# Performance work log

Hardware: AMD Instinct MI355X
Metric: run time of the kernel (lower is better)

## Reference

```python
import jax, jax.numpy as jnp
import numpy as np

B, S, DIM = 2, 4096, 768
G = DIM // 3          # gate_dim = 256
H, DK = 4, G // 4     # heads=4, d_k=64
SCALE = 1.0 / np.sqrt(DK)


def setup_inputs() -> dict:
    key = jax.random.key(0)
    ks = jax.random.split(key, 9)
    r = lambda k, shp, s: (jax.random.normal(k, shp, dtype=jnp.float32) * s)
    w_s = 1.0 / np.sqrt(G)
    return {
        "x": r(ks[0], (B, S, DIM), 1.0),
        "wq": r(ks[1], (G, G), w_s), "bq": r(ks[2], (G,), 0.01),
        "wk": r(ks[3], (G, G), w_s), "bk": r(ks[4], (G,), 0.01),
        "wv": r(ks[5], (G, G), w_s), "bv": r(ks[6], (G,), 0.01),
        "wo": r(ks[7], (G, G), w_s), "bo": r(ks[8], (G,), 0.01),
    }


def reference(x, wq, bq, wk, bk, wv, bv, wo, bo):
    # chunk(3, dim=-1): q/k/v slices of width G
    xq, xk, xv = x[..., :G], x[..., G:2 * G], x[..., 2 * G:3 * G]
    # linear projections then split into heads: [b, s, h, d]
    q = (xq @ wq.T + bq).reshape(B, S, H, DK)
    k = (xk @ wk.T + bk).reshape(B, S, H, DK)
    v = (xv @ wv.T + bv).reshape(B, S, H, DK)
    scores = jnp.einsum('bihd,bjhd->bijh', q, k) * SCALE  # [b, i, j, h]
    # NOTE: original applies Softmax(dim=1) -> over the QUERY axis i
    attn = jax.nn.softmax(scores, axis=1)
    out = jnp.einsum('bijh,bjhd->bihd', attn, v).reshape(B, S, G)
    return out @ wo.T + bo
```

## Files before the change

kernel.cpp:

```cpp
#include <hip/hip_runtime.h>

#define SEQ   4096
#define HH    4
#define SCALE 0.125f
#define SC2   0.18033688011112042f
#define C16   -23.083120654223414f

typedef __bf16 bf16x8 __attribute__((ext_vector_type(8)));
typedef __bf16 bf16x4 __attribute__((ext_vector_type(4)));
typedef float  f32x4  __attribute__((ext_vector_type(4)));

constexpr size_t OFF_W16  = 0;
constexpr size_t OFF_A    = 131072;
constexpr size_t OFF_AO   = 294912;
constexpr size_t OFF_X16  = 9732096;
constexpr size_t OFF_Q16  = 12877824;
constexpr size_t K16OFF   = 2097152;
constexpr size_t V16OFF   = 4194304;
constexpr size_t OFF_PZ   = 16023552;

__device__ __forceinline__ f32x4 mf(bf16x8 a, bf16x8 b, f32x4 c) {
    return __builtin_amdgcn_mfma_f32_16x16x32_bf16(a, b, c, 0, 0, 0);
}

__device__ __forceinline__ void gload16(const __bf16* g, __bf16* l) {
    __builtin_amdgcn_global_load_lds(
        (const __attribute__((address_space(1))) unsigned int*)g,
        (__attribute__((address_space(3))) unsigned int*)l, 16, 0, 0);
}

__device__ __forceinline__ float ex2(float x) {
    return __builtin_amdgcn_exp2f(x);
}

__global__ void k_prep(const float* __restrict__ x,
                       const float* __restrict__ wq, const float* __restrict__ wk,
                       const float* __restrict__ wv, const float* __restrict__ wo,
                       float* __restrict__ ws) {
    int bx = blockIdx.x, t = threadIdx.x;
    if (bx < 6144) {
        size_t i4 = ((size_t)bx * 256 + t) * 4;
        float4 v = *(const float4*)(x + i4);
        bf16x4 o = {(__bf16)v.x, (__bf16)v.y, (__bf16)v.z, (__bf16)v.w};
        *(bf16x4*)((__bf16*)(ws + OFF_X16) + i4) = o;
    } else if (bx < 6400) {
        int q = bx - 6144;
        int y = q >> 6;
        const float* src = (y == 0) ? wq : (y == 1) ? wk : (y == 2) ? wv : wo;
        size_t i4 = ((size_t)(q & 63) * 256 + t) * 4;
        float4 v = *(const float4*)(src + i4);
        bf16x4 o = {(__bf16)v.x, (__bf16)v.y, (__bf16)v.z, (__bf16)v.w};
        *(bf16x4*)((__bf16*)(ws + OFF_W16) + (size_t)y * 65536 + i4) = o;
    } else {
        size_t i4 = ((size_t)(bx - 6400) * 256 + t) * 4;
        *(float4*)(ws + OFF_AO + i4) = make_float4(0.f, 0.f, 0.f, 0.f);
    }
}

__global__ __launch_bounds__(256) void k_qkv_mfma(const float* __restrict__ bq,
                                                  const float* __restrict__ bk,
                                                  const float* __restrict__ bv,
                                                  float* __restrict__ ws) {
    int t = threadIdx.x, lane = t & 63, w = t >> 6;
    int yw = blockIdx.y;
    int row0 = blockIdx.x * 64 + w * 16;
    int mrow = lane & 15, quad = lane >> 4;
    const __bf16* X16 = (const __bf16*)(ws + OFF_X16);
    const __bf16* W16 = (const __bf16*)(ws + OFF_W16) + (size_t)yw * 65536;
    const float* bias = (yw == 0) ? bq : (yw == 1) ? bk : bv;
    __bf16* Qb = (__bf16*)(ws + OFF_Q16);
    f32x4 acc[16];
#pragma unroll
    for (int n = 0; n < 16; n++) acc[n] = {0.f, 0.f, 0.f, 0.f};
    const __bf16* ap = X16 + (size_t)(row0 + mrow) * 768 + yw * 256 + quad * 8;
    const __bf16* bp = W16 + (size_t)mrow * 256 + quad * 8;
    for (int kc = 0; kc < 256; kc += 32) {
        bf16x8 a = *(const bf16x8*)(ap + kc);
#pragma unroll
        for (int nt = 0; nt < 16; nt++) {
            bf16x8 b = *(const bf16x8*)(bp + (size_t)nt * 16 * 256 + kc);
            acc[nt] = mf(a, b, acc[nt]);
        }
    }
#pragma unroll
    for (int nt = 0; nt < 16; nt++) {
        int n = nt * 16 + mrow;
        float bb = bias[n];
        int h = n >> 6, d = n & 63;
#pragma unroll
        for (int r = 0; r < 4; r++) {
            int sg = row0 + quad * 4 + r;
            int b_ = sg >> 12, s = sg & 4095;
            int bh = b_ * HH + h;
            float val = acc[nt][r] + bb;
            if (yw == 0) {
                int tile = s >> 4, m = s & 15, frag = d >> 5, q2 = (d >> 3) & 3, e = d & 7;
                size_t idx = (((size_t)bh * 256 + tile) * 2 + frag) * 512 +
                             (size_t)(q2 * 16 + m) * 8 + e;
                Qb[idx] = (__bf16)val;
            } else if (yw == 1) {
                int jc = s >> 5, jj = s & 31;
                int tl = (jj >> 2) & 1, m = ((jj >> 3) << 2) | (jj & 3);
                int frag = d >> 5, q2 = (d >> 3) & 3, e = d & 7;
                size_t idx = (((size_t)bh * 128 + jc) * 4 + tl * 2 + frag) * 512 +
                             (size_t)(q2 * 16 + m) * 8 + e;
                Qb[K16OFF + idx] = (__bf16)val;
            } else {
                int jc = s >> 5, qk = (s >> 3) & 3, e = s & 7;
                int nd = d >> 4, nl = d & 15;
                size_t idx = (((size_t)bh * 128 + jc) * 4 + nd) * 512 +
                             (size_t)(qk * 16 + nl) * 8 + e;
                Qb[V16OFF + idx] = (__bf16)val;
            }
        }
    }
}

__global__ __launch_bounds__(256) void k_colstats(float* __restrict__ ws) {
    __shared__ __bf16 qbuf[2][4096];
    int t = threadIdx.x, lane = t & 63, w = t >> 6;
    int jb = blockIdx.x, iy = blockIdx.y, bh = blockIdx.z;
    int jc = jb * 4 + w;
    const __bf16* Qp = (const __bf16*)(ws + OFF_Q16);
    const __bf16* Kp = Qp + K16OFF;
    const __bf16* kb = Kp + ((size_t)(bh * 128 + jc) * 4) * 512 + lane * 8;
    bf16x8 bk00 = *(const bf16x8*)(kb);
    bf16x8 bk01 = *(const bf16x8*)(kb + 512);
    bf16x8 bk10 = *(const bf16x8*)(kb + 1024);
    bf16x8 bk11 = *(const bf16x8*)(kb + 1536);
    const __bf16* q0 = Qp + ((size_t)(bh * 256 + iy * 32) * 2) * 512 +
                       w * 1024 + lane * 8;
    gload16(q0, qbuf[0] + w * 1024);
    gload16(q0 + 512, qbuf[0] + w * 1024 + 512);
    __syncthreads();
    float z0 = 0.f, z1 = 0.f;
    for (int ic = 0; ic < 8; ic++) {
        const __bf16* cur = qbuf[ic & 1];
        if (ic < 7) {
            const __bf16* qn = Qp + ((size_t)(bh * 256 + iy * 32 + (ic + 1) * 4) * 2) * 512 +
                               w * 1024 + lane * 8;
            gload16(qn, qbuf[(ic + 1) & 1] + w * 1024);
            gload16(qn + 512, qbuf[(ic + 1) & 1] + w * 1024 + 512);
        }
#pragma unroll
        for (int it = 0; it < 4; it++) {
            bf16x8 a0 = *(const bf16x8*)(cur + it * 1024 + lane * 8);
            bf16x8 a1 = *(const bf16x8*)(cur + it * 1024 + 512 + lane * 8);
            f32x4 c0 = {0.f, 0.f, 0.f, 0.f};
            c0 = mf(a0, bk00, c0);
            c0 = mf(a1, bk01, c0);
            f32x4 c1 = {0.f, 0.f, 0.f, 0.f};
            c1 = mf(a0, bk10, c1);
            c1 = mf(a1, bk11, c1);
#pragma unroll
            for (int r = 0; r < 4; r++) {
                z0 += ex2(fmaf(c0[r], SC2, C16));
                z1 += ex2(fmaf(c1[r], SC2, C16));
            }
        }
        __syncthreads();
    }
    z0 += __shfl_xor(z0, 16, 64);
    z0 += __shfl_xor(z0, 32, 64);
    z1 += __shfl_xor(z1, 16, 64);
    z1 += __shfl_xor(z1, 32, 64);
    if (lane < 16) {
        size_t o = OFF_PZ + (size_t)iy * 32768 + (size_t)bh * SEQ +
                   jc * 32 + ((lane >> 2) << 3) + (lane & 3);
        ws[o] = z0;
        ws[o + 4] = z1;
    }
}

__global__ void k_afin(float* __restrict__ ws) {
    int idx = blockIdx.x * 256 + threadIdx.x;
    const float* pz = ws + OFF_PZ;
    float Z = 0.f;
#pragma unroll
    for (int y = 0; y < 8; y++) Z += pz[(size_t)y * 32768 + idx];
    ws[OFF_A + idx] = C16 - __log2f(Z);
}

__global__ __launch_bounds__(256) void k_attnpv(float* __restrict__ ws) {
    __shared__ __align__(16) char pool[20480];
    __bf16* ldsK = (__bf16*)pool;
    __bf16* ldsV = (__bf16*)(pool + 8192);
    float*  sA   = (float*)(pool + 16384);
    int t = threadIdx.x, lane = t & 63, w = t >> 6;
    int jy = blockIdx.y, bh = blockIdx.z;
    int it0 = blockIdx.x * 4 + w;
    int i0 = it0 * 16;
    int mrow = lane & 15, quad = lane >> 4;
    const __bf16* Qp = (const __bf16*)(ws + OFF_Q16);
    const __bf16* Kp = Qp + K16OFF;
    const __bf16* Vp = Qp + V16OFF;
    int jbase = jy * 1024;
    {
        const float* Ag = ws + OFF_A + (size_t)bh * SEQ + jbase;
        *(float4*)(sA + t * 4) = *(const float4*)(Ag + t * 4);
    }
    const __bf16* qb = Qp + ((size_t)(bh * 256 + it0) * 2) * 512 + lane * 8;
    bf16x8 aq0 = *(const bf16x8*)(qb);
    bf16x8 aq1 = *(const bf16x8*)(qb + 512);
    f32x4 oaccT[4];
#pragma unroll
    for (int nd = 0; nd < 4; nd++) oaccT[nd] = {0.f, 0.f, 0.f, 0.f};
    int c0g = jy * 32;
    {
        const __bf16* kg = Kp + ((size_t)(bh * 128 + c0g) * 4) * 512 + w * 512 + lane * 8;
        gload16(kg, ldsK + w * 512);
        const __bf16* vg = Vp + ((size_t)(bh * 128 + c0g) * 4) * 512 + w * 512 + lane * 8;
        gload16(vg, ldsV + w * 512);
    }
    __syncthreads();

    for (int jt = 0; jt < 32; jt++) {
        const __bf16* curK = ldsK + (jt & 1) * 2048;
        const __bf16* curV = ldsV + (jt & 1) * 2048;
        if (jt < 31) {
            int cn = c0g + jt + 1;
            const __bf16* kg = Kp + ((size_t)(bh * 128 + cn) * 4) * 512 + w * 512 + lane * 8;
            gload16(kg, ldsK + ((jt + 1) & 1) * 2048 + w * 512);
            const __bf16* vg = Vp + ((size_t)(bh * 128 + cn) * 4) * 512 + w * 512 + lane * 8;
            gload16(vg, ldsV + ((jt + 1) & 1) * 2048 + w * 512);
        }
        f32x4 a4L = *(const f32x4*)(sA + jt * 32 + quad * 8);
        f32x4 a4H = *(const f32x4*)(sA + jt * 32 + quad * 8 + 4);
        bf16x8 ck0 = *(const bf16x8*)(curK + lane * 8);
        bf16x8 ck1 = *(const bf16x8*)(curK + 512 + lane * 8);
        bf16x8 ck2 = *(const bf16x8*)(curK + 1024 + lane * 8);
        bf16x8 ck3 = *(const bf16x8*)(curK + 1536 + lane * 8);
        f32x4 cT0 = {0.f, 0.f, 0.f, 0.f};
        cT0 = mf(ck0, aq0, cT0);
        cT0 = mf(ck1, aq1, cT0);
        f32x4 cT1 = {0.f, 0.f, 0.f, 0.f};
        cT1 = mf(ck2, aq0, cT1);
        cT1 = mf(ck3, aq1, cT1);
        bf16x8 pb;
#pragma unroll
        for (int r = 0; r < 4; r++) {
            pb[r]     = (__bf16)ex2(fmaf(cT0[r], SC2, a4L[r]));
            pb[4 + r] = (__bf16)ex2(fmaf(cT1[r], SC2, a4H[r]));
        }
#pragma unroll
        for (int nd = 0; nd < 4; nd++) {
            bf16x8 bv = *(const bf16x8*)(curV + nd * 512 + lane * 8);
            oaccT[nd] = mf(bv, pb, oaccT[nd]);
        }
        __syncthreads();
    }

    float* sO = (float*)pool + (size_t)w * (16 * 65);
#pragma unroll
    for (int nd = 0; nd < 4; nd++)
#pragma unroll
        for (int r = 0; r < 4; r++)
            sO[mrow * 65 + nd * 16 + quad * 4 + r] = oaccT[nd][r];
    int b = bh >> 2, h = bh & 3;
    float* AO = ws + OFF_AO;
#pragma unroll
    for (int c = 0; c < 16; c++) {
        atomicAdd(&AO[((size_t)(b * SEQ + i0 + c)) * 256 + h * 64 + lane],
                  sO[c * 65 + lane]);
    }
}

__global__ __launch_bounds__(256) void k_outproj_mfma(const float* __restrict__ bo,
                                                      float* __restrict__ ws,
                                                      float* __restrict__ out) {
    int t = threadIdx.x, lane = t & 63, w = t >> 6;
    int row0 = blockIdx.x * 64 + w * 16;
    int mrow = lane & 15, quad = lane >> 4;
    const float* AO = ws + OFF_AO;
    const __bf16* W16 = (const __bf16*)(ws + OFF_W16) + (size_t)3 * 65536;
    f32x4 acc[16];
#pragma unroll
    for (int n = 0; n < 16; n++) acc[n] = {0.f, 0.f, 0.f, 0.f};
    const float* ap = AO + (size_t)(row0 + mrow) * 256 + quad * 8;
    const __bf16* bp = W16 + (size_t)mrow * 256 + quad * 8;
    for (int kc = 0; kc < 256; kc += 32) {
        float4 u = *(const float4*)(ap + kc);
        float4 v = *(const float4*)(ap + kc + 4);
        bf16x8 a = {(__bf16)u.x, (__bf16)u.y, (__bf16)u.z, (__bf16)u.w,
                    (__bf16)v.x, (__bf16)v.y, (__bf16)v.z, (__bf16)v.w};
#pragma unroll
        for (int nt = 0; nt < 16; nt++) {
            bf16x8 b = *(const bf16x8*)(bp + (size_t)nt * 16 * 256 + kc);
            acc[nt] = mf(a, b, acc[nt]);
        }
    }
#pragma unroll
    for (int nt = 0; nt < 16; nt++) {
        int n = nt * 16 + mrow;
        float bb = bo[n];
#pragma unroll
        for (int r = 0; r < 4; r++) {
            int sg = row0 + quad * 4 + r;
            out[(size_t)sg * 256 + n] = acc[nt][r] + bb;
        }
    }
}

extern "C" void kernel_launch(void* const* d_in, const int* in_sizes, int n_in,
                              void* d_out, int out_size, void* d_ws, size_t ws_size,
                              hipStream_t stream) {
    const float* x  = (const float*)d_in[0];
    const float* wq = (const float*)d_in[1];
    const float* bq = (const float*)d_in[2];
    const float* wk = (const float*)d_in[3];
    const float* bk = (const float*)d_in[4];
    const float* wv = (const float*)d_in[5];
    const float* bv = (const float*)d_in[6];
    const float* wo = (const float*)d_in[7];
    const float* bo = (const float*)d_in[8];
    float* ws = (float*)d_ws;
    float* out = (float*)d_out;

    k_prep<<<8448, 256, 0, stream>>>(x, wq, wk, wv, wo, ws);
    k_qkv_mfma<<<dim3(128, 3), 256, 0, stream>>>(bq, bk, bv, ws);
    k_colstats<<<dim3(32, 8, 8), 256, 0, stream>>>(ws);
    k_afin<<<128, 256, 0, stream>>>(ws);
    k_attnpv<<<dim3(64, 4, 8), 256, 0, stream>>>(ws);
    k_outproj_mfma<<<128, 256, 0, stream>>>(bo, ws, out);
}
```

Baseline: 224.7 us.

## Fold softmax scale into Wq, seed MFMA accumulators with offsets, widen attnpv tiles

Pre-multiplies Wq and bq by the log2-scaled softmax factor so the score MFMAs directly produce exp2 arguments. The column offset (C16 or the per-column log-sum A) is passed in as the MFMA accumulator seed, which removes the per-element fma. k_attnpv now handles two 16-row query tiles per wave, reusing each K/V LDS fragment twice, and reads A straight from global with prefetch instead of staging it in LDS. The QKV and out-projection kernels are split along N into more blocks to raise occupancy and parallelism. Rounding the pre-scaled Wq to bf16 shifts numerics slightly, and halving the attnpv grid reduces block count.

```diff
diff --git a/kernel.cpp b/kernel.cpp
--- a/kernel.cpp
+++ b/kernel.cpp
@@ -47,9 +47,11 @@
         int q = bx - 6144;
         int y = q >> 6;
         const float* src = (y == 0) ? wq : (y == 1) ? wk : (y == 2) ? wv : wo;
+        float sc = (y == 0) ? SC2 : 1.0f;
         size_t i4 = ((size_t)(q & 63) * 256 + t) * 4;
         float4 v = *(const float4*)(src + i4);
-        bf16x4 o = {(__bf16)v.x, (__bf16)v.y, (__bf16)v.z, (__bf16)v.w};
+        bf16x4 o = {(__bf16)(v.x * sc), (__bf16)(v.y * sc),
+                    (__bf16)(v.z * sc), (__bf16)(v.w * sc)};
         *(bf16x4*)((__bf16*)(ws + OFF_W16) + (size_t)y * 65536 + i4) = o;
     } else {
         size_t i4 = ((size_t)(bx - 6400) * 256 + t) * 4;
@@ -63,29 +65,31 @@
                                                   float* __restrict__ ws) {
     int t = threadIdx.x, lane = t & 63, w = t >> 6;
     int yw = blockIdx.y;
+    int ntb = blockIdx.z * 8;
     int row0 = blockIdx.x * 64 + w * 16;
     int mrow = lane & 15, quad = lane >> 4;
     const __bf16* X16 = (const __bf16*)(ws + OFF_X16);
     const __bf16* W16 = (const __bf16*)(ws + OFF_W16) + (size_t)yw * 65536;
     const float* bias = (yw == 0) ? bq : (yw == 1) ? bk : bv;
     __bf16* Qb = (__bf16*)(ws + OFF_Q16);
-    f32x4 acc[16];
-#pragma unroll
-    for (int n = 0; n < 16; n++) acc[n] = {0.f, 0.f, 0.f, 0.f};
+    f32x4 acc[8];
+#pragma unroll
+    for (int n = 0; n < 8; n++) acc[n] = {0.f, 0.f, 0.f, 0.f};
     const __bf16* ap = X16 + (size_t)(row0 + mrow) * 768 + yw * 256 + quad * 8;
-    const __bf16* bp = W16 + (size_t)mrow * 256 + quad * 8;
+    const __bf16* bp = W16 + (size_t)ntb * 4096 + (size_t)mrow * 256 + quad * 8;
     for (int kc = 0; kc < 256; kc += 32) {
         bf16x8 a = *(const bf16x8*)(ap + kc);
 #pragma unroll
-        for (int nt = 0; nt < 16; nt++) {
-            bf16x8 b = *(const bf16x8*)(bp + (size_t)nt * 16 * 256 + kc);
+        for (int nt = 0; nt < 8; nt++) {
+            bf16x8 b = *(const bf16x8*)(bp + (size_t)nt * 4096 + kc);
             acc[nt] = mf(a, b, acc[nt]);
         }
     }
 #pragma unroll
-    for (int nt = 0; nt < 16; nt++) {
-        int n = nt * 16 + mrow;
+    for (int nt = 0; nt < 8; nt++) {
+        int n = (ntb + nt) * 16 + mrow;
         float bb = bias[n];
+        if (yw == 0) bb *= SC2;
         int h = n >> 6, d = n & 63;
 #pragma unroll
         for (int r = 0; r < 4; r++) {
@@ -133,6 +137,7 @@
     gload16(q0, qbuf[0] + w * 1024);
     gload16(q0 + 512, qbuf[0] + w * 1024 + 512);
     __syncthreads();
+    const f32x4 cin = {C16, C16, C16, C16};
     float z0 = 0.f, z1 = 0.f;
     for (int ic = 0; ic < 8; ic++) {
         const __bf16* cur = qbuf[ic & 1];
@@ -146,16 +151,14 @@
         for (int it = 0; it < 4; it++) {
             bf16x8 a0 = *(const bf16x8*)(cur + it * 1024 + lane * 8);
             bf16x8 a1 = *(const bf16x8*)(cur + it * 1024 + 512 + lane * 8);
-            f32x4 c0 = {0.f, 0.f, 0.f, 0.f};
-            c0 = mf(a0, bk00, c0);
+            f32x4 c0 = mf(a0, bk00, cin);
             c0 = mf(a1, bk01, c0);
-            f32x4 c1 = {0.f, 0.f, 0.f, 0.f};
-            c1 = mf(a0, bk10, c1);
+            f32x4 c1 = mf(a0, bk10, cin);
             c1 = mf(a1, bk11, c1);
 #pragma unroll
             for (int r = 0; r < 4; r++) {
-                z0 += ex2(fmaf(c0[r], SC2, C16));
-                z1 += ex2(fmaf(c1[r], SC2, C16));
+                z0 += ex2(c0[r]);
+                z1 += ex2(c1[r]);
             }
         }
         __syncthreads();
@@ -182,87 +185,100 @@
 }
 
 __global__ __launch_bounds__(256) void k_attnpv(float* __restrict__ ws) {
-    __shared__ __align__(16) char pool[20480];
+    __shared__ __align__(16) char pool[17408];
     __bf16* ldsK = (__bf16*)pool;
     __bf16* ldsV = (__bf16*)(pool + 8192);
-    float*  sA   = (float*)(pool + 16384);
     int t = threadIdx.x, lane = t & 63, w = t >> 6;
     int jy = blockIdx.y, bh = blockIdx.z;
-    int it0 = blockIdx.x * 4 + w;
-    int i0 = it0 * 16;
+    int itp = blockIdx.x * 4 + w;
+    int it0 = itp * 2;
     int mrow = lane & 15, quad = lane >> 4;
     const __bf16* Qp = (const __bf16*)(ws + OFF_Q16);
     const __bf16* Kp = Qp + K16OFF;
     const __bf16* Vp = Qp + V16OFF;
-    int jbase = jy * 1024;
-    {
-        const float* Ag = ws + OFF_A + (size_t)bh * SEQ + jbase;
-        *(float4*)(sA + t * 4) = *(const float4*)(Ag + t * 4);
-    }
+    const float* Ag = ws + OFF_A + (size_t)bh * SEQ + jy * 1024 + quad * 8;
+
     const __bf16* qb = Qp + ((size_t)(bh * 256 + it0) * 2) * 512 + lane * 8;
-    bf16x8 aq0 = *(const bf16x8*)(qb);
-    bf16x8 aq1 = *(const bf16x8*)(qb + 512);
-    f32x4 oaccT[4];
-#pragma unroll
-    for (int nd = 0; nd < 4; nd++) oaccT[nd] = {0.f, 0.f, 0.f, 0.f};
+    bf16x8 aq00 = *(const bf16x8*)(qb);
+    bf16x8 aq01 = *(const bf16x8*)(qb + 512);
+    bf16x8 aq10 = *(const bf16x8*)(qb + 1024);
+    bf16x8 aq11 = *(const bf16x8*)(qb + 1536);
+
+    f32x4 oT0[4], oT1[4];
+#pragma unroll
+    for (int nd = 0; nd < 4; nd++) {
+        oT0[nd] = {0.f, 0.f, 0.f, 0.f};
+        oT1[nd] = {0.f, 0.f, 0.f, 0.f};
+    }
     int c0g = jy * 32;
-    {
-        const __bf16* kg = Kp + ((size_t)(bh * 128 + c0g) * 4) * 512 + w * 512 + lane * 8;
-        gload16(kg, ldsK + w * 512);
-        const __bf16* vg = Vp + ((size_t)(bh * 128 + c0g) * 4) * 512 + w * 512 + lane * 8;
-        gload16(vg, ldsV + w * 512);
-    }
+    const __bf16* kg = Kp + ((size_t)(bh * 128 + c0g) * 4) * 512 + w * 512 + lane * 8;
+    const __bf16* vg = Vp + ((size_t)(bh * 128 + c0g) * 4) * 512 + w * 512 + lane * 8;
+    gload16(kg, ldsK + w * 512);
+    gload16(vg, ldsV + w * 512);
+    kg += 2048; vg += 2048;
+    f32x4 aL = *(const f32x4*)(Ag);
+    f32x4 aH = *(const f32x4*)(Ag + 4);
     __syncthreads();
 
     for (int jt = 0; jt < 32; jt++) {
         const __bf16* curK = ldsK + (jt & 1) * 2048;
         const __bf16* curV = ldsV + (jt & 1) * 2048;
+        f32x4 aLn = aL, aHn = aH;
         if (jt < 31) {
-            int cn = c0g + jt + 1;
-            const __bf16* kg = Kp + ((size_t)(bh * 128 + cn) * 4) * 512 + w * 512 + lane * 8;
             gload16(kg, ldsK + ((jt + 1) & 1) * 2048 + w * 512);
-            const __bf16* vg = Vp + ((size_t)(bh * 128 + cn) * 4) * 512 + w * 512 + lane * 8;
             gload16(vg, ldsV + ((jt + 1) & 1) * 2048 + w * 512);
-        }
-        f32x4 a4L = *(const f32x4*)(sA + jt * 32 + quad * 8);
-        f32x4 a4H = *(const f32x4*)(sA + jt * 32 + quad * 8 + 4);
+            kg += 2048; vg += 2048;
+            aLn = *(const f32x4*)(Ag + (jt + 1) * 32);
+            aHn = *(const f32x4*)(Ag + (jt + 1) * 32 + 4);
+        }
         bf16x8 ck0 = *(const bf16x8*)(curK + lane * 8);
         bf16x8 ck1 = *(const bf16x8*)(curK + 512 + lane * 8);
         bf16x8 ck2 = *(const bf16x8*)(curK + 1024 + lane * 8);
         bf16x8 ck3 = *(const bf16x8*)(curK + 1536 + lane * 8);
-        f32x4 cT0 = {0.f, 0.f, 0.f, 0.f};
-        cT0 = mf(ck0, aq0, cT0);
-        cT0 = mf(ck1, aq1, cT0);
-        f32x4 cT1 = {0.f, 0.f, 0.f, 0.f};
-        cT1 = mf(ck2, aq0, cT1);
-        cT1 = mf(ck3, aq1, cT1);
-        bf16x8 pb;
+        f32x4 c00 = mf(ck0, aq00, aL); c00 = mf(ck1, aq01, c00);
+        f32x4 c01 = mf(ck2, aq00, aH); c01 = mf(ck3, aq01, c01);
+        f32x4 c10 = mf(ck0, aq10, aL); c10 = mf(ck1, aq11, c10);
+        f32x4 c11 = mf(ck2, aq10, aH); c11 = mf(ck3, aq11, c11);
+        bf16x8 pb0, pb1;
 #pragma unroll
         for (int r = 0; r < 4; r++) {
-            pb[r]     = (__bf16)ex2(fmaf(cT0[r], SC2, a4L[r]));
-            pb[4 + r] = (__bf16)ex2(fmaf(cT1[r], SC2, a4H[r]));
+            pb0[r]     = (__bf16)ex2(c00[r]);
+            pb0[4 + r] = (__bf16)ex2(c01[r]);
+            pb1[r]     = (__bf16)ex2(c10[r]);
+            pb1[4 + r] = (__bf16)ex2(c11[r]);
         }
 #pragma unroll
         for (int nd = 0; nd < 4; nd++) {
             bf16x8 bv = *(const bf16x8*)(curV + nd * 512 + lane * 8);
-            oaccT[nd] = mf(bv, pb, oaccT[nd]);
-        }
+            oT0[nd] = mf(bv, pb0, oT0[nd]);
+            oT1[nd] = mf(bv, pb1, oT1[nd]);
+        }
+        aL = aLn; aH = aHn;
         __syncthreads();
     }
 
-    float* sO = (float*)pool + (size_t)w * (16 * 65);
-#pragma unroll
-    for (int nd = 0; nd < 4; nd++)
-#pragma unroll
-        for (int r = 0; r < 4; r++)
-            sO[mrow * 65 + nd * 16 + quad * 4 + r] = oaccT[nd][r];
+    float* sO = (float*)pool + (size_t)w * 1040;
     int b = bh >> 2, h = bh & 3;
     float* AO = ws + OFF_AO;
-#pragma unroll
-    for (int c = 0; c < 16; c++) {
+    int i0 = it0 * 16;
+#pragma unroll
+    for (int nd = 0; nd < 4; nd++)
+#pragma unroll
+        for (int r = 0; r < 4; r++)
+            sO[mrow * 65 + nd * 16 + quad * 4 + r] = oT0[nd][r];
+#pragma unroll
+    for (int c = 0; c < 16; c++)
         atomicAdd(&AO[((size_t)(b * SEQ + i0 + c)) * 256 + h * 64 + lane],
                   sO[c * 65 + lane]);
-    }
+#pragma unroll
+    for (int nd = 0; nd < 4; nd++)
+#pragma unroll
+        for (int r = 0; r < 4; r++)
+            sO[mrow * 65 + nd * 16 + quad * 4 + r] = oT1[nd][r];
+#pragma unroll
+    for (int c = 0; c < 16; c++)
+        atomicAdd(&AO[((size_t)(b * SEQ + i0 + 16 + c)) * 256 + h * 64 + lane],
+                  sO[c * 65 + lane]);
 }
 
 __global__ __launch_bounds__(256) void k_outproj_mfma(const float* __restrict__ bo,
@@ -270,28 +286,29 @@
                                                       float* __restrict__ out) {
     int t = threadIdx.x, lane = t & 63, w = t >> 6;
     int row0 = blockIdx.x * 64 + w * 16;
+    int ntb = blockIdx.y * 4;
     int mrow = lane & 15, quad = lane >> 4;
     const float* AO = ws + OFF_AO;
     const __bf16* W16 = (const __bf16*)(ws + OFF_W16) + (size_t)3 * 65536;
-    f32x4 acc[16];
-#pragma unroll
-    for (int n = 0; n < 16; n++) acc[n] = {0.f, 0.f, 0.f, 0.f};
+    f32x4 acc[4];
+#pragma unroll
+    for (int n = 0; n < 4; n++) acc[n] = {0.f, 0.f, 0.f, 0.f};
     const float* ap = AO + (size_t)(row0 + mrow) * 256 + quad * 8;
-    const __bf16* bp = W16 + (size_t)mrow * 256 + quad * 8;
+    const __bf16* bp = W16 + (size_t)ntb * 4096 + (size_t)mrow * 256 + quad * 8;
     for (int kc = 0; kc < 256; kc += 32) {
         float4 u = *(const float4*)(ap + kc);
         float4 v = *(const float4*)(ap + kc + 4);
         bf16x8 a = {(__bf16)u.x, (__bf16)u.y, (__bf16)u.z, (__bf16)u.w,
                     (__bf16)v.x, (__bf16)v.y, (__bf16)v.z, (__bf16)v.w};
 #pragma unroll
-        for (int nt = 0; nt < 16; nt++) {
-            bf16x8 b = *(const bf16x8*)(bp + (size_t)nt * 16 * 256 + kc);
+        for (int nt = 0; nt < 4; nt++) {
+            bf16x8 b = *(const bf16x8*)(bp + (size_t)nt * 4096 + kc);
             acc[nt] = mf(a, b, acc[nt]);
         }
     }
 #pragma unroll
-    for (int nt = 0; nt < 16; nt++) {
-        int n = nt * 16 + mrow;
+    for (int nt = 0; nt < 4; nt++) {
+        int n = (ntb + nt) * 16 + mrow;
         float bb = bo[n];
 #pragma unroll
         for (int r = 0; r < 4; r++) {
@@ -317,9 +334,9 @@
     float* out = (float*)d_out;
 
     k_prep<<<8448, 256, 0, stream>>>(x, wq, wk, wv, wo, ws);
-    k_qkv_mfma<<<dim3(128, 3), 256, 0, stream>>>(bq, bk, bv, ws);
+    k_qkv_mfma<<<dim3(128, 3, 2), 256, 0, stream>>>(bq, bk, bv, ws);
     k_colstats<<<dim3(32, 8, 8), 256, 0, stream>>>(ws);
     k_afin<<<128, 256, 0, stream>>>(ws);
-    k_attnpv<<<dim3(64, 4, 8), 256, 0, stream>>>(ws);
-    k_outproj_mfma<<<128, 256, 0, stream>>>(bo, ws, out);
-}
+    k_attnpv<<<dim3(32, 4, 8), 256, 0, stream>>>(ws);
+    k_outproj_mfma<<<dim3(128, 4), 256, 0, stream>>>(bo, ws, out);
+}
```

New measurement: 213.5 us. 1.05x faster.
